# Kernel optimization log

Hardware: AMD Instinct MI355X
Metric: run time of the kernel (lower is better)

## Reference

```python
import jax, jax.numpy as jnp
import numpy as np

B, P, C, O = 64, 8732, 81, 16
THRESH = 0.5
NEGPOS = 3
VAR0, VAR1 = 0.1, 0.2


def setup_inputs() -> dict:
    key = jax.random.key(0)
    k1, k2, k3, k4, k5, k6, k7 = jax.random.split(key, 7)
    # ground-truth boxes in point form (xmin,ymin,xmax,ymax), valid and inside [0,1]
    lo = jax.random.uniform(k1, (B, O, 2), minval=0.0, maxval=0.7)
    wh = jax.random.uniform(k2, (B, O, 2), minval=0.05, maxval=0.3)
    truths = jnp.concatenate([lo, lo + wh], axis=-1)
    labels = jax.random.randint(k3, (B, O), 0, C - 1).astype(jnp.int32)
    # prior boxes in center-size form with strictly positive w/h
    ctr = jax.random.uniform(k4, (P, 2), minval=0.05, maxval=0.95)
    pwh = jax.random.uniform(k5, (P, 2), minval=0.05, maxval=0.5)
    dbox = jnp.concatenate([ctr, pwh], axis=-1)
    loc_data = jax.random.normal(k6, (B, P, 4), dtype=jnp.float32)
    conf_data = jax.random.normal(k7, (B, P, C), dtype=jnp.float32)
    return {"loc_data": loc_data, "conf_data": conf_data, "dbox": dbox,
            "truths": truths, "labels": labels}


def point_form(boxes):
    return jnp.concatenate([boxes[:, :2] - boxes[:, 2:] / 2,
                            boxes[:, :2] + boxes[:, 2:] / 2], axis=1)


def jaccard(box_a, box_b):
    # box_a: [A,4], box_b: [B,4] point form -> IoU [A,B]
    max_xy = jnp.minimum(box_a[:, None, 2:], box_b[None, :, 2:])
    min_xy = jnp.maximum(box_a[:, None, :2], box_b[None, :, :2])
    inter = jnp.prod(jnp.clip(max_xy - min_xy, 0.0, None), axis=-1)  # [A,B]
    area_a = jnp.prod(box_a[:, 2:] - box_a[:, :2], axis=-1)[:, None]
    area_b = jnp.prod(box_b[:, 2:] - box_b[:, :2], axis=-1)[None, :]
    return inter / (area_a + area_b - inter)


def encode(matched, priors):
    g_cxcy = ((matched[:, :2] + matched[:, 2:]) / 2 - priors[:, :2]) / (VAR0 * priors[:, 2:])
    g_wh = jnp.log((matched[:, 2:] - matched[:, :2]) / priors[:, 2:]) / VAR1
    return jnp.concatenate([g_cxcy, g_wh], axis=1)


def match_one(truths, labels, priors, priors_pf):
    overlaps = jaccard(truths, priors_pf)                  # [O, P]
    best_prior_idx = jnp.argmax(overlaps, axis=1)          # [O]
    best_truth_overlap = jnp.max(overlaps, axis=0)         # [P]
    best_truth_idx = jnp.argmax(overlaps, axis=0)          # [P]
    best_truth_overlap = best_truth_overlap.at[best_prior_idx].set(2.0)
    best_truth_idx = best_truth_idx.at[best_prior_idx].set(jnp.arange(truths.shape[0]))
    matches = truths[best_truth_idx]                       # [P,4]
    conf = jnp.where(best_truth_overlap < THRESH, 0, labels[best_truth_idx] + 1)
    loc = encode(matches, priors)                          # [P,4]
    return loc, conf


def reference(loc_data, conf_data, dbox, truths, labels):
    priors_pf = point_form(dbox)
    loc_t, conf_t = jax.vmap(match_one, in_axes=(0, 0, None, None))(
        truths, labels, dbox, priors_pf)                   # [B,P,4], [B,P]

    pos_mask = conf_t > 0                                  # [B,P]
    # localization smooth-L1 (beta=1) over positive priors
    d = jnp.abs(loc_data - loc_t)
    sl1 = jnp.where(d < 1.0, 0.5 * d * d, d - 0.5)
    loss_l = jnp.sum(sl1 * pos_mask[..., None].astype(sl1.dtype))

    # per-prior cross entropy
    logz = jax.nn.logsumexp(conf_data, axis=-1)            # [B,P]
    picked = jnp.take_along_axis(conf_data, conf_t[..., None], axis=-1)[..., 0]
    ce = logz - picked                                     # [B,P]

    # hard negative mining: rank negatives by CE (positives zeroed)
    loss_c_neg = jnp.where(pos_mask, 0.0, ce)
    order = jnp.argsort(-loss_c_neg, axis=1)
    idx_rank = jnp.argsort(order, axis=1)
    num_pos = jnp.sum(pos_mask, axis=1, keepdims=True)     # [B,1]
    num_neg = jnp.clip(num_pos * NEGPOS, None, P)
    neg_mask = idx_rank < num_neg

    sel = (pos_mask | neg_mask).astype(ce.dtype)
    loss_c = jnp.sum(ce * sel)

    N = jnp.sum(num_pos).astype(loss_l.dtype)
    return loss_l / N, loss_c / N
```

## Files before the change

### kernel.cpp

```cpp
#include <hip/hip_runtime.h>
#include <stdint.h>
#include <math.h>

#define B 64
#define P 8732
#define C 81
#define O 16
#define THRESH 0.5f
#define NEGPOS 3
#define VAR0 0.1f
#define VAR1 0.2f

#define ITER 8
#define ROWS_PER_WAVE (4 * ITER)
#define ROWS_PER_BLOCK (4 * ROWS_PER_WAVE)

__global__ void init_k(int* __restrict__ num_pos, float* __restrict__ possum,
                       float* __restrict__ lossl, float* __restrict__ acc) {
    int i = threadIdx.x;
    if (i < B) { num_pos[i] = 0; possum[i] = 0.f; lossl[i] = 0.f; }
    if (i < 2) acc[i] = 0.f;
}

__global__ __launch_bounds__(1024) void bp_k(const float* __restrict__ dbox,
                                             const float* __restrict__ truths,
                                             int* __restrict__ forced_p) {
    const int b = blockIdx.x;
    const int tid = threadIdx.x;
    const int lane = tid & 63;
    const int o = tid >> 6;
    const float tx0 = truths[(b * O + o) * 4 + 0];
    const float ty0 = truths[(b * O + o) * 4 + 1];
    const float tx1 = truths[(b * O + o) * 4 + 2];
    const float ty1 = truths[(b * O + o) * 4 + 3];
    const float ta = (tx1 - tx0) * (ty1 - ty0);

    unsigned long long best = 0ull;
    for (int p = lane; p < P; p += 64) {
        const float4 db = *(const float4*)(dbox + (size_t)p * 4);
        const float px0 = db.x - db.z * 0.5f, py0 = db.y - db.w * 0.5f;
        const float px1 = db.x + db.z * 0.5f, py1 = db.y + db.w * 0.5f;
        const float parea = (px1 - px0) * (py1 - py0);
        float ix = fminf(tx1, px1) - fmaxf(tx0, px0);
        float iy = fminf(ty1, py1) - fmaxf(ty0, py0);
        ix = fmaxf(ix, 0.f); iy = fmaxf(iy, 0.f);
        const float inter = ix * iy;
        const float ov = inter / (ta + parea - inter);
        const unsigned long long key =
            ((unsigned long long)__float_as_uint(ov) << 32) |
            (unsigned long long)(0xFFFFFFFFu - (unsigned)p);
        if (key > best) best = key;
    }
    for (int off = 32; off; off >>= 1) {
        const unsigned long long o2 = __shfl_xor(best, off);
        if (o2 > best) best = o2;
    }
    if (lane == 0)
        forced_p[b * O + o] = (int)(0xFFFFFFFFu - (unsigned)(best & 0xFFFFFFFFull));
}

__global__ __launch_bounds__(256) void loss_k(
        const float* __restrict__ loc_data,
        const float* __restrict__ conf_data,
        const float* __restrict__ dbox,
        const float* __restrict__ truths,
        const int* __restrict__ labels,
        const int* __restrict__ forced_p,
        float* __restrict__ negce,
        int* __restrict__ num_pos, float* __restrict__ possum,
        float* __restrict__ lossl) {
    const int b = blockIdx.y;
    const int tid = threadIdx.x;
    const int lane = tid & 63;
    const int wid = tid >> 6;
    const int sub = lane & 15;
    const int g = lane >> 4;

    __shared__ float s_truth[O * 4];
    __shared__ int s_fp[O];
    __shared__ int s_lab[O];
    __shared__ float s_l, s_p;
    __shared__ int s_n;
    if (tid < O * 4) s_truth[tid] = truths[b * O * 4 + tid];
    if (tid < O) { s_fp[tid] = forced_p[b * O + tid]; s_lab[tid] = labels[b * O + tid]; }
    if (tid == 0) { s_l = 0.f; s_p = 0.f; s_n = 0; }
    __syncthreads();

    const float tx0 = s_truth[sub * 4 + 0], ty0 = s_truth[sub * 4 + 1];
    const float tx1 = s_truth[sub * 4 + 2], ty1 = s_truth[sub * 4 + 3];
    const float tarea = (tx1 - tx0) * (ty1 - ty0);
    const int myfp = s_fp[sub];

    float l_acc = 0.f;
    float p_acc = 0.f;
    int n_acc = 0;

    const int wbase = blockIdx.x * ROWS_PER_BLOCK + wid * ROWS_PER_WAVE;

    for (int r = 0; r < ITER; ++r) {
        const int p = wbase + 4 * r + g;
        const bool active = (p < P);
        const int pc = active ? p : P - 1;
        const size_t row = (size_t)b * P + pc;

        const float4 db = *(const float4*)(dbox + (size_t)pc * 4);
        const float cx = db.x, cy = db.y, w = db.z, h = db.w;
        const float px0 = cx - w * 0.5f, py0 = cy - h * 0.5f;
        const float px1 = cx + w * 0.5f, py1 = cy + h * 0.5f;
        const float parea = (px1 - px0) * (py1 - py0);

        float ix = fminf(tx1, px1) - fmaxf(tx0, px0);
        float iy = fminf(ty1, py1) - fmaxf(ty0, py0);
        ix = fmaxf(ix, 0.f); iy = fmaxf(iy, 0.f);
        const float inter = ix * iy;
        float ov = inter / (tarea + parea - inter);
        int ti = sub;
        for (int off = 8; off; off >>= 1) {
            const float o2 = __shfl_xor(ov, off);
            const int i2 = __shfl_xor(ti, off);
            if (o2 > ov || (o2 == ov && i2 < ti)) { ov = o2; ti = i2; }
        }
        const unsigned long long bal = __ballot(active && (myfp == pc));
        const unsigned mask16 = (unsigned)((bal >> (16 * g)) & 0xFFFFull);
        if (mask16 != 0u) { ti = 31 - __clz(mask16); ov = 2.0f; }
        const int conf = (ov < THRESH) ? 0 : (s_lab[ti] + 1);
        const bool pos = conf > 0;

        const float* rp = conf_data + row * C;
        float v[6];
#pragma unroll
        for (int j = 0; j < 5; ++j) v[j] = rp[sub + 16 * j];
        const float v80 = rp[80];
        v[5] = (sub == 0) ? v80 : -INFINITY;

        float m = v[0];
#pragma unroll
        for (int j = 1; j < 6; ++j) m = fmaxf(m, v[j]);
        for (int off = 8; off; off >>= 1) m = fmaxf(m, __shfl_xor(m, off));

        float s = 0.f, pk = 0.f;
#pragma unroll
        for (int j = 0; j < 5; ++j) {
            s += expf(v[j] - m);
            pk += (sub + 16 * j == conf) ? v[j] : 0.f;
        }
        s += expf(v[5] - m);
        if (sub == 0 && conf == 80) pk = v80;
        for (int off = 8; off; off >>= 1) {
            s += __shfl_xor(s, off);
            pk += __shfl_xor(pk, off);
        }
        const float cev = (logf(s) + m) - pk;

        if (active && sub == 0) {
            negce[row] = pos ? 0.f : cev;
            if (pos) { p_acc += cev; n_acc++; }
        }
        if (active && pos && sub < 4) {
            const float mx0 = s_truth[ti * 4 + 0];
            const float my0 = s_truth[ti * 4 + 1];
            const float mx1 = s_truth[ti * 4 + 2];
            const float my1 = s_truth[ti * 4 + 3];
            float tgt;
            if (sub == 0)      tgt = ((mx0 + mx1) * 0.5f - cx) / (VAR0 * w);
            else if (sub == 1) tgt = ((my0 + my1) * 0.5f - cy) / (VAR0 * h);
            else if (sub == 2) tgt = logf((mx1 - mx0) / w) / VAR1;
            else               tgt = logf((my1 - my0) / h) / VAR1;
            const float d = fabsf(loc_data[row * 4 + sub] - tgt);
            l_acc += (d < 1.f) ? 0.5f * d * d : d - 0.5f;
        }
    }
    for (int off = 32; off; off >>= 1) {
        l_acc += __shfl_xor(l_acc, off);
        p_acc += __shfl_xor(p_acc, off);
        n_acc += __shfl_xor(n_acc, off);
    }
    if (lane == 0) {
        atomicAdd(&s_l, l_acc);
        atomicAdd(&s_p, p_acc);
        atomicAdd(&s_n, n_acc);
    }
    __syncthreads();
    if (tid == 0) {
        atomicAdd(&lossl[b], s_l);
        atomicAdd(&possum[b], s_p);
        atomicAdd(&num_pos[b], s_n);
    }
}

__global__ __launch_bounds__(1024) void mine_k(
        const float* __restrict__ negce,
        const int* __restrict__ num_pos,
        const float* __restrict__ possum,
        float* __restrict__ acc) {
    const int b = blockIdx.x;
    const int tid = threadIdx.x;
    const int lane = tid & 63;
    const int wid = tid >> 6;
    const float* x = negce + (size_t)b * P;
    float v[9];
#pragma unroll
    for (int j = 0; j < 9; ++j) {
        const int i = tid + j * 1024;
        v[j] = (i < P) ? x[i] : -1.0f;
    }
    int k = num_pos[b] * NEGPOS;
    if (k > P) k = P;

    __shared__ int wred[2][16];
    __shared__ float wsumf[16];
    __shared__ int wcnt[16];
    float S = 0.f;
    if (k > 0) {
        unsigned lo = 0u, hi = 0x7F800000u;
        int parity = 0;
        while (lo < hi) {
            const unsigned mid = lo + ((hi - lo) >> 1);
            const float t = __uint_as_float(mid);
            int cnt = 0;
#pragma unroll
            for (int j = 0; j < 9; ++j) cnt += (v[j] > t) ? 1 : 0;
            for (int off = 32; off; off >>= 1) cnt += __shfl_xor(cnt, off);
            if (lane == 0) wred[parity][wid] = cnt;
            __syncthreads();
            int total = 0;
#pragma unroll
            for (int w = 0; w < 16; ++w) total += wred[parity][w];
            if (total < k) hi = mid; else lo = mid + 1;
            parity ^= 1;
        }
        const float t = __uint_as_float(lo);
        float sum = 0.f;
        int cnt = 0;
#pragma unroll
        for (int j = 0; j < 9; ++j) {
            if (v[j] > t) { sum += v[j]; cnt++; }
        }
        for (int off = 32; off; off >>= 1) {
            sum += __shfl_xor(sum, off);
            cnt += __shfl_xor(cnt, off);
        }
        if (lane == 0) { wsumf[wid] = sum; wcnt[wid] = cnt; }
        __syncthreads();
        if (tid == 0) {
            float ts = 0.f; int tc = 0;
#pragma unroll
            for (int w = 0; w < 16; ++w) { ts += wsumf[w]; tc += wcnt[w]; }
            S = ts + (float)(k - tc) * t;
        }
    }
    if (tid == 0) atomicAdd(&acc[1], possum[b] + S);
}

__global__ void final_k(const float* __restrict__ acc,
                        const int* __restrict__ num_pos,
                        const float* __restrict__ lossl,
                        float* __restrict__ out) {
    float N = 0.f, L = 0.f;
    for (int b = 0; b < B; ++b) { N += (float)num_pos[b]; L += lossl[b]; }
    out[0] = L / N;
    out[1] = acc[1] / N;
}

extern "C" void kernel_launch(void* const* d_in, const int* in_sizes, int n_in,
                              void* d_out, int out_size, void* d_ws, size_t ws_size,
                              hipStream_t stream) {
    (void)in_sizes; (void)n_in; (void)out_size; (void)ws_size;
    const float* loc_data  = (const float*)d_in[0];
    const float* conf_data = (const float*)d_in[1];
    const float* dbox      = (const float*)d_in[2];
    const float* truths    = (const float*)d_in[3];
    const int*   labels    = (const int*)d_in[4];
    float* out = (float*)d_out;

    int* forced_p = (int*)d_ws;
    float* negce  = (float*)(forced_p + B * O);
    int* num_pos  = (int*)(negce + (size_t)B * P);
    float* possum = (float*)(num_pos + B);
    float* lossl  = possum + B;
    float* acc    = lossl + B;

    init_k<<<1, 256, 0, stream>>>(num_pos, possum, lossl, acc);
    bp_k<<<B, 1024, 0, stream>>>(dbox, truths, forced_p);
    loss_k<<<dim3((P + ROWS_PER_BLOCK - 1) / ROWS_PER_BLOCK, B), 256, 0, stream>>>(
        loc_data, conf_data, dbox, truths, labels, forced_p,
        negce, num_pos, possum, lossl);
    mine_k<<<B, 1024, 0, stream>>>(negce, num_pos, possum, acc);
    final_k<<<1, 1, 0, stream>>>(acc, num_pos, lossl, out);
}
```

Baseline: 379.8 us.

## Stage conf rows in LDS, two lanes per prior, fold init and final kernels

The loss kernel now copies each wave's 32-row chunk of conf_data into shared memory with coalesced float4 loads. Each prior is then handled by two lanes that split the 16 truths and the 81 classes, which replaces the 16-lane shuffle reductions. The init kernel is folded into bp_k and the final kernel into mine_k through a last-block-done counter, saving two launches. The cost is about 41KB of LDS per block, which may limit occupancy, plus serial per-lane loops over about 40 classes with strided LDS reads that can hit bank conflicts.

```diff
diff --git a/kernel.cpp b/kernel.cpp
--- a/kernel.cpp
+++ b/kernel.cpp
@@ -11,22 +11,25 @@
 #define VAR0 0.1f
 #define VAR1 0.2f
 
-#define ITER 8
-#define ROWS_PER_WAVE (4 * ITER)
-#define ROWS_PER_BLOCK (4 * ROWS_PER_WAVE)
-
-__global__ void init_k(int* __restrict__ num_pos, float* __restrict__ possum,
-                       float* __restrict__ lossl, float* __restrict__ acc) {
-    int i = threadIdx.x;
-    if (i < B) { num_pos[i] = 0; possum[i] = 0.f; lossl[i] = 0.f; }
-    if (i < 2) acc[i] = 0.f;
-}
+#define CHR 32
+#define CPB 4
+#define GRIDX ((P + CHR * CPB - 1) / (CHR * CPB))
 
 __global__ __launch_bounds__(1024) void bp_k(const float* __restrict__ dbox,
                                              const float* __restrict__ truths,
-                                             int* __restrict__ forced_p) {
+                                             int* __restrict__ forced_p,
+                                             int* __restrict__ num_pos,
+                                             float* __restrict__ possum,
+                                             float* __restrict__ lossl,
+                                             float* __restrict__ acc,
+                                             int* __restrict__ done) {
     const int b = blockIdx.x;
     const int tid = threadIdx.x;
+    if (b == 0) {
+        if (tid < B) { num_pos[tid] = 0; possum[tid] = 0.f; lossl[tid] = 0.f; }
+        if (tid == B) { acc[0] = 0.f; acc[1] = 0.f; }
+        if (tid == B + 1) { *done = 0; }
+    }
     const int lane = tid & 63;
     const int o = tid >> 6;
     const float tx0 = truths[(b * O + o) * 4 + 0];
@@ -69,105 +72,105 @@
         float* __restrict__ negce,
         int* __restrict__ num_pos, float* __restrict__ possum,
         float* __restrict__ lossl) {
+    __shared__ __align__(16) float sbuf[CPB][CHR * C];
+    __shared__ float s_truth[O * 4];
+    __shared__ int s_fp[O];
+    __shared__ int s_lab[O];
+
     const int b = blockIdx.y;
     const int tid = threadIdx.x;
     const int lane = tid & 63;
     const int wid = tid >> 6;
-    const int sub = lane & 15;
-    const int g = lane >> 4;
-
-    __shared__ float s_truth[O * 4];
-    __shared__ int s_fp[O];
-    __shared__ int s_lab[O];
-    __shared__ float s_l, s_p;
-    __shared__ int s_n;
     if (tid < O * 4) s_truth[tid] = truths[b * O * 4 + tid];
     if (tid < O) { s_fp[tid] = forced_p[b * O + tid]; s_lab[tid] = labels[b * O + tid]; }
-    if (tid == 0) { s_l = 0.f; s_p = 0.f; s_n = 0; }
+
+    const int chunk = blockIdx.x * CPB + wid;
+    const int p0 = chunk * CHR;
+    const int nrows = (p0 < P) ? min(CHR, P - p0) : 0;
+
+    if (nrows > 0) {
+        const int quads = (nrows * C) >> 2;
+        const float4* g = (const float4*)(conf_data + ((size_t)b * P + p0) * C);
+        float4* l = (float4*)(&sbuf[wid][0]);
+        for (int q = lane; q < quads; q += 64) l[q] = g[q];
+    }
     __syncthreads();
 
-    const float tx0 = s_truth[sub * 4 + 0], ty0 = s_truth[sub * 4 + 1];
-    const float tx1 = s_truth[sub * 4 + 2], ty1 = s_truth[sub * 4 + 3];
-    const float tarea = (tx1 - tx0) * (ty1 - ty0);
-    const int myfp = s_fp[sub];
-
-    float l_acc = 0.f;
-    float p_acc = 0.f;
+    const int half = lane & 1;
+    const int r = lane >> 1;
+    const int row_p = p0 + r;
+    float l_acc = 0.f, p_acc = 0.f;
     int n_acc = 0;
 
-    const int wbase = blockIdx.x * ROWS_PER_BLOCK + wid * ROWS_PER_WAVE;
-
-    for (int r = 0; r < ITER; ++r) {
-        const int p = wbase + 4 * r + g;
-        const bool active = (p < P);
-        const int pc = active ? p : P - 1;
-        const size_t row = (size_t)b * P + pc;
-
-        const float4 db = *(const float4*)(dbox + (size_t)pc * 4);
-        const float cx = db.x, cy = db.y, w = db.z, h = db.w;
-        const float px0 = cx - w * 0.5f, py0 = cy - h * 0.5f;
-        const float px1 = cx + w * 0.5f, py1 = cy + h * 0.5f;
+    if (nrows > 0 && r < nrows) {
+        const float4 db = *(const float4*)(dbox + (size_t)row_p * 4);
+        const float px0 = db.x - db.z * 0.5f, py0 = db.y - db.w * 0.5f;
+        const float px1 = db.x + db.z * 0.5f, py1 = db.y + db.w * 0.5f;
         const float parea = (px1 - px0) * (py1 - py0);
 
-        float ix = fminf(tx1, px1) - fmaxf(tx0, px0);
-        float iy = fminf(ty1, py1) - fmaxf(ty0, py0);
-        ix = fmaxf(ix, 0.f); iy = fmaxf(iy, 0.f);
-        const float inter = ix * iy;
-        float ov = inter / (tarea + parea - inter);
-        int ti = sub;
-        for (int off = 8; off; off >>= 1) {
-            const float o2 = __shfl_xor(ov, off);
-            const int i2 = __shfl_xor(ti, off);
-            if (o2 > ov || (o2 == ov && i2 < ti)) { ov = o2; ti = i2; }
-        }
-        const unsigned long long bal = __ballot(active && (myfp == pc));
-        const unsigned mask16 = (unsigned)((bal >> (16 * g)) & 0xFFFFull);
-        if (mask16 != 0u) { ti = 31 - __clz(mask16); ov = 2.0f; }
-        const int conf = (ov < THRESH) ? 0 : (s_lab[ti] + 1);
+        float ov = -1.f;
+        int ti = 0;
+#pragma unroll
+        for (int j = 0; j < 8; ++j) {
+            const int o = half * 8 + j;
+            const float tx0 = s_truth[o * 4 + 0], ty0 = s_truth[o * 4 + 1];
+            const float tx1 = s_truth[o * 4 + 2], ty1 = s_truth[o * 4 + 3];
+            float ix = fminf(tx1, px1) - fmaxf(tx0, px0);
+            float iy = fminf(ty1, py1) - fmaxf(ty0, py0);
+            ix = fmaxf(ix, 0.f); iy = fmaxf(iy, 0.f);
+            const float inter = ix * iy;
+            const float ta = (tx1 - tx0) * (ty1 - ty0);
+            const float v = inter / (ta + parea - inter);
+            if (v > ov) { ov = v; ti = o; }
+        }
+        unsigned long long key =
+            ((unsigned long long)__float_as_uint(ov) << 32) |
+            (unsigned long long)(unsigned)(O - 1 - ti);
+        const unsigned long long ko = __shfl_xor(key, 1);
+        if (ko > key) key = ko;
+        ov = __uint_as_float((unsigned)(key >> 32));
+        ti = (O - 1) - (int)(key & 0xFFFFFFFFull);
+        bool forced = false;
+#pragma unroll
+        for (int o = 0; o < O; ++o)
+            if (s_fp[o] == row_p) { ti = o; forced = true; }
+        const int conf = (forced || ov >= THRESH) ? (s_lab[ti] + 1) : 0;
         const bool pos = conf > 0;
 
-        const float* rp = conf_data + row * C;
-        float v[6];
-#pragma unroll
-        for (int j = 0; j < 5; ++j) v[j] = rp[sub + 16 * j];
-        const float v80 = rp[80];
-        v[5] = (sub == 0) ? v80 : -INFINITY;
-
-        float m = v[0];
-#pragma unroll
-        for (int j = 1; j < 6; ++j) m = fmaxf(m, v[j]);
-        for (int off = 8; off; off >>= 1) m = fmaxf(m, __shfl_xor(m, off));
-
+        const float* rowb = &sbuf[wid][r * C];
+        const int c0 = half * 41;
+        const int nc = half ? 40 : 41;
+        float m = -INFINITY;
+        for (int c = 0; c < nc; ++c) m = fmaxf(m, rowb[c0 + c]);
+        m = fmaxf(m, __shfl_xor(m, 1));
         float s = 0.f, pk = 0.f;
-#pragma unroll
-        for (int j = 0; j < 5; ++j) {
-            s += expf(v[j] - m);
-            pk += (sub + 16 * j == conf) ? v[j] : 0.f;
-        }
-        s += expf(v[5] - m);
-        if (sub == 0 && conf == 80) pk = v80;
-        for (int off = 8; off; off >>= 1) {
-            s += __shfl_xor(s, off);
-            pk += __shfl_xor(pk, off);
-        }
+        for (int c = 0; c < nc; ++c) {
+            const float v = rowb[c0 + c];
+            s += expf(v - m);
+            if (c0 + c == conf) pk = v;
+        }
+        s += __shfl_xor(s, 1);
+        pk += __shfl_xor(pk, 1);
         const float cev = (logf(s) + m) - pk;
 
-        if (active && sub == 0) {
-            negce[row] = pos ? 0.f : cev;
-            if (pos) { p_acc += cev; n_acc++; }
-        }
-        if (active && pos && sub < 4) {
-            const float mx0 = s_truth[ti * 4 + 0];
-            const float my0 = s_truth[ti * 4 + 1];
-            const float mx1 = s_truth[ti * 4 + 2];
-            const float my1 = s_truth[ti * 4 + 3];
-            float tgt;
-            if (sub == 0)      tgt = ((mx0 + mx1) * 0.5f - cx) / (VAR0 * w);
-            else if (sub == 1) tgt = ((my0 + my1) * 0.5f - cy) / (VAR0 * h);
-            else if (sub == 2) tgt = logf((mx1 - mx0) / w) / VAR1;
-            else               tgt = logf((my1 - my0) / h) / VAR1;
-            const float d = fabsf(loc_data[row * 4 + sub] - tgt);
-            l_acc += (d < 1.f) ? 0.5f * d * d : d - 0.5f;
+        if (half == 0) {
+            negce[(size_t)b * P + row_p] = pos ? 0.f : cev;
+            if (pos) {
+                p_acc = cev; n_acc = 1;
+                const float mx0 = s_truth[ti * 4 + 0], my0 = s_truth[ti * 4 + 1];
+                const float mx1 = s_truth[ti * 4 + 2], my1 = s_truth[ti * 4 + 3];
+                const float4 ld = *(const float4*)(loc_data + ((size_t)b * P + row_p) * 4);
+                const float t0 = ((mx0 + mx1) * 0.5f - db.x) / (VAR0 * db.z);
+                const float t1 = ((my0 + my1) * 0.5f - db.y) / (VAR0 * db.w);
+                const float t2 = logf((mx1 - mx0) / db.z) / VAR1;
+                const float t3 = logf((my1 - my0) / db.w) / VAR1;
+                const float d0 = fabsf(ld.x - t0), d1 = fabsf(ld.y - t1);
+                const float d2 = fabsf(ld.z - t2), d3 = fabsf(ld.w - t3);
+                l_acc = ((d0 < 1.f) ? 0.5f * d0 * d0 : d0 - 0.5f)
+                      + ((d1 < 1.f) ? 0.5f * d1 * d1 : d1 - 0.5f)
+                      + ((d2 < 1.f) ? 0.5f * d2 * d2 : d2 - 0.5f)
+                      + ((d3 < 1.f) ? 0.5f * d3 * d3 : d3 - 0.5f);
+            }
         }
     }
     for (int off = 32; off; off >>= 1) {
@@ -176,15 +179,9 @@
         n_acc += __shfl_xor(n_acc, off);
     }
     if (lane == 0) {
-        atomicAdd(&s_l, l_acc);
-        atomicAdd(&s_p, p_acc);
-        atomicAdd(&s_n, n_acc);
-    }
-    __syncthreads();
-    if (tid == 0) {
-        atomicAdd(&lossl[b], s_l);
-        atomicAdd(&possum[b], s_p);
-        atomicAdd(&num_pos[b], s_n);
+        atomicAdd(&lossl[b], l_acc);
+        atomicAdd(&possum[b], p_acc);
+        atomicAdd(&num_pos[b], n_acc);
     }
 }
 
@@ -192,7 +189,9 @@
         const float* __restrict__ negce,
         const int* __restrict__ num_pos,
         const float* __restrict__ possum,
-        float* __restrict__ acc) {
+        const float* __restrict__ lossl,
+        float* __restrict__ acc, int* __restrict__ done,
+        float* __restrict__ out) {
     const int b = blockIdx.x;
     const int tid = threadIdx.x;
     const int lane = tid & 63;
@@ -249,17 +248,19 @@
             S = ts + (float)(k - tc) * t;
         }
     }
-    if (tid == 0) atomicAdd(&acc[1], possum[b] + S);
-}
-
-__global__ void final_k(const float* __restrict__ acc,
-                        const int* __restrict__ num_pos,
-                        const float* __restrict__ lossl,
-                        float* __restrict__ out) {
-    float N = 0.f, L = 0.f;
-    for (int b = 0; b < B; ++b) { N += (float)num_pos[b]; L += lossl[b]; }
-    out[0] = L / N;
-    out[1] = acc[1] / N;
+    if (tid == 0) {
+        atomicAdd(&acc[1], possum[b] + S);
+        __threadfence();
+        const int prev = atomicAdd(done, 1);
+        if (prev == B - 1) {
+            __threadfence();
+            float N = 0.f, L = 0.f;
+            for (int i = 0; i < B; ++i) { N += (float)num_pos[i]; L += lossl[i]; }
+            const float cval = atomicAdd(&acc[1], 0.0f);
+            out[0] = L / N;
+            out[1] = cval / N;
+        }
+    }
 }
 
 extern "C" void kernel_launch(void* const* d_in, const int* in_sizes, int n_in,
@@ -279,12 +280,12 @@
     float* possum = (float*)(num_pos + B);
     float* lossl  = possum + B;
     float* acc    = lossl + B;
-
-    init_k<<<1, 256, 0, stream>>>(num_pos, possum, lossl, acc);
-    bp_k<<<B, 1024, 0, stream>>>(dbox, truths, forced_p);
-    loss_k<<<dim3((P + ROWS_PER_BLOCK - 1) / ROWS_PER_BLOCK, B), 256, 0, stream>>>(
+    int* done     = (int*)(acc + 2);
+
+    bp_k<<<B, 1024, 0, stream>>>(dbox, truths, forced_p,
+                                 num_pos, possum, lossl, acc, done);
+    loss_k<<<dim3(GRIDX, B), 256, 0, stream>>>(
         loc_data, conf_data, dbox, truths, labels, forced_p,
         negce, num_pos, possum, lossl);
-    mine_k<<<B, 1024, 0, stream>>>(negce, num_pos, possum, acc);
-    final_k<<<1, 1, 0, stream>>>(acc, num_pos, lossl, out);
-}
+    mine_k<<<B, 1024, 0, stream>>>(negce, num_pos, possum, lossl, acc, done, out);
+}
```

Measured after the change: 485.0 us. +27.7%, slower.
